# Kernel optimization log

Measured on AMD Instinct MI355X. Metric: run time of the kernel, lower is better.

Reference implementation:

```python
import jax, jax.numpy as jnp
import numpy as np
from jax import lax

EPS = 1e-5
NUM_GROUPS = 32
OFFSET_SCALE = 1.0
K = 3            # deformable conv kernel size
KK = K * K
DWK = 7          # depthwise kernel size for offset predictor


def group_norm(x, gamma, beta, num_groups=NUM_GROUPS):
    B, C, H, W = x.shape
    xg = x.reshape(B, num_groups, C // num_groups, H, W)
    m = xg.mean(axis=(2, 3, 4), keepdims=True)
    v = xg.var(axis=(2, 3, 4), keepdims=True)
    xn = ((xg - m) * lax.rsqrt(v + EPS)).reshape(B, C, H, W)
    return xn * gamma[None, :, None, None] + beta[None, :, None, None]


def bilinear_gather(x, py, px):
    # x: [B,C,H,W]; py, px: [B,KK,H,W] absolute sample coords -> [B,C,KK,H,W]
    B, C, H, W = x.shape
    y0 = jnp.floor(py)
    x0 = jnp.floor(px)
    wy1 = py - y0
    wx1 = px - x0
    wy0 = 1.0 - wy1
    wx0 = 1.0 - wx1
    xf = x.reshape(B, C, H * W)

    def gather(yi, xi):
        valid = (yi >= 0) & (yi <= H - 1) & (xi >= 0) & (xi <= W - 1)
        yc = jnp.clip(yi, 0, H - 1).astype(jnp.int32)
        xc = jnp.clip(xi, 0, W - 1).astype(jnp.int32)
        idx = (yc * W + xc).reshape(B, -1)                      # [B, KK*H*W]
        g = jax.vmap(lambda a, i: a[:, i])(xf, idx)             # [B, C, KK*H*W]
        g = g.reshape(B, C, KK, H, W)
        return g * valid.astype(x.dtype)[:, None]

    out = (gather(y0, x0) * (wy0 * wx0)[:, None]
           + gather(y0, x0 + 1.0) * (wy0 * wx1)[:, None]
           + gather(y0 + 1.0, x0) * (wy1 * wx0)[:, None]
           + gather(y0 + 1.0, x0 + 1.0) * (wy1 * wx1)[:, None])
    return out


def deform_conv(x, dw, pw, pwb, w, b):
    # x: [B,C,H,W]; dw: [C,1,DWK,DWK] depthwise; pw: [2*KK,C,1,1]; w: [O,C,K,K]
    B, C, H, W = x.shape
    dn = ('NCHW', 'OIHW', 'NCHW')
    f = lax.conv_general_dilated(x, dw, (1, 1), 'SAME',
                                 feature_group_count=C, dimension_numbers=dn)
    off = lax.conv_general_dilated(f, pw, (1, 1), 'SAME', dimension_numbers=dn)
    off = (off + pwb[None, :, None, None]) * OFFSET_SCALE       # [B,2*KK,H,W]
    off = off.reshape(B, KK, 2, H, W)
    ks = jnp.arange(K, dtype=x.dtype) - (K - 1) / 2             # [-1,0,1]
    ky = jnp.repeat(ks, K)                                      # [KK]
    kx = jnp.tile(ks, K)
    yy, xx = jnp.meshgrid(jnp.arange(H, dtype=x.dtype),
                          jnp.arange(W, dtype=x.dtype), indexing='ij')
    py = yy[None, None] + ky[None, :, None, None] + off[:, :, 0]  # [B,KK,H,W]
    px = xx[None, None] + kx[None, :, None, None] + off[:, :, 1]
    sampled = bilinear_gather(x, py, px)                        # [B,C,KK,H,W]
    O = w.shape[0]
    out = jnp.einsum('bckhw,ock->bohw', sampled, w.reshape(O, C, KK))
    return out + b[None, :, None, None]


def setup_inputs() -> dict:
    key = jax.random.key(0)
    ks = jax.random.split(key, 10)
    B, C, H, W = 4, 256, 64, 64
    O = C
    x = jax.random.normal(ks[0], (B, C, H, W), dtype=jnp.float32)

    def conv_w(k, shape, fan_in):
        return jax.random.normal(k, shape, dtype=jnp.float32) / np.sqrt(fan_in)

    inp = {
        'x': x,
        'gn1_g': jnp.ones((C,), jnp.float32), 'gn1_b': jnp.zeros((C,), jnp.float32),
        'dw1': conv_w(ks[1], (C, 1, DWK, DWK), DWK * DWK),
        'pw1': jax.random.normal(ks[2], (2 * KK, C, 1, 1), jnp.float32) * 0.01,
        'pwb1': jnp.zeros((2 * KK,), jnp.float32),
        'w1': conv_w(ks[3], (O, C, K, K), C * KK),
        'b1': jnp.zeros((O,), jnp.float32),
        'gn2_g': jnp.ones((O,), jnp.float32), 'gn2_b': jnp.zeros((O,), jnp.float32),
        'dw2': conv_w(ks[4], (O, 1, DWK, DWK), DWK * DWK),
        'pw2': jax.random.normal(ks[5], (2 * KK, O, 1, 1), jnp.float32) * 0.01,
        'pwb2': jnp.zeros((2 * KK,), jnp.float32),
        'w2': conv_w(ks[6], (O, O, K, K), O * KK),
        'b2': jnp.zeros((O,), jnp.float32),
    }
    return inp


def reference(x, gn1_g, gn1_b, dw1, pw1, pwb1, w1, b1,
              gn2_g, gn2_b, dw2, pw2, pwb2, w2, b2):
    h = jax.nn.relu(group_norm(x, gn1_g, gn1_b))
    h = deform_conv(h, dw1, pw1, pwb1, w1, b1)
    h = jax.nn.relu(group_norm(h, gn2_g, gn2_b))
    # Dropout / DropPath are identity in eval mode
    h = deform_conv(h, dw2, pw2, pwb2, w2, b2)
    return h + x  # shortcut is Identity (in_channels == out_channels)
```

## Files before the change

kernel.cpp:

```cpp
#include <hip/hip_runtime.h>

#define B_    4
#define C_    256
#define H_    64
#define W_    64
#define HW_   4096
#define NG_   32
#define CPG_  8
#define KK_   9
#define NOFF_ 18

typedef __attribute__((ext_vector_type(8))) short short8;
typedef __attribute__((ext_vector_type(4))) short short4v;
typedef __attribute__((ext_vector_type(4))) float floatx4;
typedef __attribute__((ext_vector_type(16))) float floatx16;

static __device__ __forceinline__ short f2bf(float f) {
    union { float f; unsigned u; } v; v.f = f;
    unsigned r = v.u + 0x7fff + ((v.u >> 16) & 1);
    return (short)(r >> 16);
}
static __device__ __forceinline__ float bf2f(short s) {
    union { unsigned u; float f; } v;
    v.u = ((unsigned)(unsigned short)s) << 16;
    return v.f;
}
static __device__ __forceinline__ unsigned pkbf(float lo, float hi) {
    unsigned r;
    asm("v_cvt_pk_bf16_f32 %0, %1, %2" : "=v"(r) : "v"(lo), "v"(hi));
    return r;
}

__global__ __launch_bounds__(1024) void gn_relu_f32_kernel(
    const float* __restrict__ in, const float* __restrict__ gamma,
    const float* __restrict__ beta, short* __restrict__ outb)
{
    __shared__ float cache[32768];
    __shared__ float red[32];
    __shared__ float sh_rs, sh_m;
    int b = blockIdx.x >> 5;
    int g = blockIdx.x & 31;
    const int N = CPG_ * HW_;
    size_t base = ((size_t)(b * C_ + g * CPG_)) * HW_;
    const float4* in4 = (const float4*)(in + base);
    int t = threadIdx.x;

    float s = 0.f, ss = 0.f;
    for (int i = t; i < N / 4; i += 1024) {
        float4 v = in4[i];
        *(float4*)&cache[i * 4] = v;
        s  += v.x + v.y + v.z + v.w;
        ss += v.x * v.x + v.y * v.y + v.z * v.z + v.w * v.w;
    }
    #pragma unroll
    for (int off = 32; off > 0; off >>= 1) {
        s  += __shfl_down(s, off, 64);
        ss += __shfl_down(ss, off, 64);
    }
    int wid = t >> 6;
    if ((t & 63) == 0) { red[wid] = s; red[16 + wid] = ss; }
    __syncthreads();
    if (t == 0) {
        float S = 0.f, SS = 0.f;
        #pragma unroll
        for (int i = 0; i < 16; ++i) { S += red[i]; SS += red[16 + i]; }
        float m = S / (float)N;
        float var = SS / (float)N - m * m;
        sh_rs = rsqrtf(var + 1e-5f);
        sh_m = m;
    }
    __syncthreads();
    float rs = sh_rs, m = sh_m;
    short4v* out4 = (short4v*)(outb + base);
    for (int i = t; i < N / 4; i += 1024) {
        int ch = g * CPG_ + (i >> 10);
        float ga = gamma[ch] * rs;
        float be = beta[ch] - m * ga;
        float4 v = *(const float4*)&cache[i * 4];
        short4v o;
        o.x = f2bf(fmaxf(fmaf(v.x, ga, be), 0.f));
        o.y = f2bf(fmaxf(fmaf(v.y, ga, be), 0.f));
        o.z = f2bf(fmaxf(fmaf(v.z, ga, be), 0.f));
        o.w = f2bf(fmaxf(fmaf(v.w, ga, be), 0.f));
        out4[i] = o;
    }
}

__global__ __launch_bounds__(256) void dw7t_tr_kernel(
    const short* __restrict__ in,
    const float* __restrict__ dwk,
    short* __restrict__ fdwt,
    short* __restrict__ ht,
    const float* __restrict__ pstats,
    const float* __restrict__ gamma, const float* __restrict__ beta)
{
    __shared__ __align__(16) char smem[78144];
    const float Ninv = 1.f / (float)(CPG_ * HW_);
    int t = threadIdx.x;
    int blk = blockIdx.x;
    if (blk < 256) {
        short (*tile)[38][72] = (short(*)[38][72])smem;
        float (*wk8)[49]      = (float(*)[49])(smem + 43776);
        short (*outs)[2048]   = (short(*)[2048])(smem + 45344);
        float* gsh            = (float*)(smem + 78112);
        int b = blk >> 6, o8 = (blk >> 1) & 31, rh = blk & 1;
        int c0 = o8 * 8;
        if (pstats && t < 64) {
            const float* pp = pstats + (((size_t)(b * 64 + t)) * 32 + o8) * 2;
            float s = pp[0], q = pp[1];
            #pragma unroll
            for (int off = 32; off > 0; off >>= 1) {
                s += __shfl_down(s, off, 64);
                q += __shfl_down(q, off, 64);
            }
            if (t == 0) {
                float m = s * Ninv;
                float var = q * Ninv - m * m;
                gsh[0] = m;
                gsh[1] = rsqrtf(var + 1e-5f);
            }
        }
        unsigned* tz = (unsigned*)smem;
        for (int i = t; i < 10944; i += 256) tz[i] = 0u;
        for (int i = t; i < 392; i += 256)
            wk8[i / 49][i % 49] = dwk[(c0 + i / 49) * 49 + (i % 49)];
        __syncthreads();
        float m_g = 0.f, rs_g = 0.f;
        if (pstats) { m_g = gsh[0]; rs_g = gsh[1]; }
        for (int ch = 0; ch < 8; ++ch) {
            const short* src = in + ((size_t)(b * C_ + c0 + ch)) * HW_;
            float ga = 0.f, be = 0.f;
            if (pstats) {
                ga = gamma[c0 + ch] * rs_g;
                be = beta[c0 + ch] - m_g * ga;
            }
            for (int i = t; i < 608; i += 256) {
                int rr = i >> 4, xq = i & 15;
                int ry = rh * 32 + rr - 3;
                if (ry >= 0 && ry < 64) {
                    short4v v = *(const short4v*)(src + ry * 64 + xq * 4);
                    if (pstats) {
                        v.x = f2bf(fmaxf(fmaf(bf2f(v.x), ga, be), 0.f));
                        v.y = f2bf(fmaxf(fmaf(bf2f(v.y), ga, be), 0.f));
                        v.z = f2bf(fmaxf(fmaf(bf2f(v.z), ga, be), 0.f));
                        v.w = f2bf(fmaxf(fmaf(bf2f(v.w), ga, be), 0.f));
                    }
                    *(short4v*)&tile[ch][rr][4 + xq * 4] = v;
                }
            }
        }
        __syncthreads();
        for (int it = 0; it < 16; ++it) {
            int q = it * 256 + t;
            int ch = q >> 9, y = (q >> 4) & 31, x0 = (q & 15) << 2;
            float a0 = 0.f, a1 = 0.f, a2 = 0.f, a3 = 0.f;
            const float* wr0 = wk8[ch];
            #pragma unroll
            for (int dy = 0; dy < 7; ++dy) {
                const short* trw = &tile[ch][y + dy][x0];
                short4v s0 = *(const short4v*)trw;
                short4v s1 = *(const short4v*)(trw + 4);
                short4v s2 = *(const short4v*)(trw + 8);
                float r[12] = {bf2f(s0.x), bf2f(s0.y), bf2f(s0.z), bf2f(s0.w),
                               bf2f(s1.x), bf2f(s1.y), bf2f(s1.z), bf2f(s1.w),
                               bf2f(s2.x), bf2f(s2.y), bf2f(s2.z), bf2f(s2.w)};
                const float* wr = wr0 + dy * 7;
                #pragma unroll
                for (int dx = 0; dx < 7; ++dx) {
                    float wv = wr[dx];
                    a0 = fmaf(r[dx + 1], wv, a0);
                    a1 = fmaf(r[dx + 2], wv, a1);
                    a2 = fmaf(r[dx + 3], wv, a2);
                    a3 = fmaf(r[dx + 4], wv, a3);
                }
            }
            short4v o;
            o.x = f2bf(a0); o.y = f2bf(a1); o.z = f2bf(a2); o.w = f2bf(a3);
            *(short4v*)&outs[ch][y * 64 + x0] = o;
        }
        __syncthreads();
        for (int it = 0; it < 8; ++it) {
            int p = it * 256 + t;
            short8 v;
            #pragma unroll
            for (int ch = 0; ch < 8; ++ch) v[ch] = outs[ch][p];
            *(short8*)(fdwt + (((size_t)(b * 64 + rh * 32 + (p >> 6)) * 32 + o8) * 64
                               + (p & 63)) * 8) = v;
        }
    } else {
        unsigned* ltile = (unsigned*)smem;
        float* gmrs = (float*)(smem + 65536);
        int q0 = blk - 256;
        int q = ((q0 & 7) << 5) | (q0 >> 3);
        int b = q >> 6;
        int px0 = (q & 63) * 64;
        const short* sb = in + (size_t)b * C_ * HW_;
        if (pstats) {
            int gq = t >> 3, rq = t & 7;
            float s = 0.f, qs = 0.f;
            for (int rr = rq; rr < 64; rr += 8) {
                const float* pp = pstats + (((size_t)(b * 64 + rr)) * 32 + gq) * 2;
                s += pp[0]; qs += pp[1];
            }
            s  += __shfl_down(s, 4, 64);  qs += __shfl_down(qs, 4, 64);
            s  += __shfl_down(s, 2, 64);  qs += __shfl_down(qs, 2, 64);
            s  += __shfl_down(s, 1, 64);  qs += __shfl_down(qs, 1, 64);
            if (rq == 0) {
                float m = s * Ninv;
                float var = qs * Ninv - m * m;
                gmrs[gq] = m;
                gmrs[32 + gq] = rsqrtf(var + 1e-5f);
            }
        }
        __syncthreads();
        int pq4 = t & 15, cphi = t >> 4;
        #pragma unroll
        for (int i = 0; i < 8; ++i) {
            int cp = i * 16 + cphi;
            const short* r0 = sb + (size_t)(2 * cp) * HW_ + px0 + pq4 * 4;
            short4v lo = *(const short4v*)r0;
            short4v hi = *(const short4v*)(r0 + HW_);
            float ga0 = 0.f, be0 = 0.f, ga1 = 0.f, be1 = 0.f;
            if (pstats) {
                int g0 = cp >> 2;
                float mm = gmrs[g0], rr2 = gmrs[32 + g0];
                ga0 = gamma[2 * cp] * rr2;     be0 = beta[2 * cp] - mm * ga0;
                ga1 = gamma[2 * cp + 1] * rr2; be1 = beta[2 * cp + 1] - mm * ga1;
            }
            #pragma unroll
            for (int j = 0; j < 4; ++j) {
                int pl = pq4 * 4 + j;
                unsigned wrd;
                if (pstats) {
                    float v0 = fmaxf(fmaf(bf2f(lo[j]), ga0, be0), 0.f);
                    float v1 = fmaxf(fmaf(bf2f(hi[j]), ga1, be1), 0.f);
                    wrd = pkbf(v0, v1);
                } else {
                    wrd = (unsigned)(unsigned short)lo[j]
                        | ((unsigned)(unsigned short)hi[j] << 16);
                }
                ltile[pl * 132 + (cp ^ ((pl & 7) << 2))] = wrd;
            }
        }
        __syncthreads();
        int co = t & 31, ph2 = t >> 5;
        #pragma unroll
        for (int r = 0; r < 8; ++r) {
            int pl = r * 8 + ph2;
            uint4 v = *(const uint4*)&ltile[pl * 132 + ((co * 4) ^ ((pl & 7) << 2))];
            *(uint4*)(ht + ((size_t)b * HW_ + px0 + pl) * C_ + co * 8) = v;
        }
    }
}

__global__ __launch_bounds__(256) void wpack_all_kernel(
    const float* __restrict__ w1, const float* __restrict__ w2,
    const float* __restrict__ pw1, const float* __restrict__ pw2,
    short* __restrict__ wp1, short* __restrict__ wp2,
    short* __restrict__ ppk1, short* __restrict__ ppk2)
{
    int blk = blockIdx.x;
    if (blk < 4608) {
        const float* w = (blk < 2304) ? w1 : w2;
        short* wp = (blk < 2304) ? wp1 : wp2;
        int src = (blk % 2304) * 256 + threadIdx.x;
        float v = w[src];
        int o = src / (C_ * KK_);
        int r = src - o * (C_ * KK_);
        int c = r / KK_;
        int g = r - c * KK_;
        int ot   = o >> 5;
        int lane = (o & 31) | (((c >> 3) & 1) << 5);
        int j    = c & 7;
        int slab = g * 16 + (c >> 4);
        wp[(slab << 12) | (ot << 9) | (lane << 3) | j] = f2bf(v);
    } else {
        int q = blk - 4608;
        const float* pw = (q < 32) ? pw1 : pw2;
        short* ppk = (q < 32) ? ppk1 : ppk2;
        int idx = (q & 31) * 256 + threadIdx.x;
        int j = idx & 7, lane = (idx >> 3) & 63;
        int ot = (idx >> 9) & 1, sl = idx >> 10;
        int o = ot * 16 + (lane & 15);
        int k = sl * 32 + (lane >> 4) * 8 + j;
        ppk[idx] = (o < NOFF_) ? f2bf(pw[o * C_ + k]) : (short)0;
    }
}

__global__ __launch_bounds__(1024, 4) void deform_fused_kernel(
    const short* __restrict__ ht,   const short* __restrict__ fdw,
    const short* __restrict__ ppk,  const float* __restrict__ pwb,
    const short* __restrict__ wp,   const float* __restrict__ bias,
    const float* __restrict__ resid, float* __restrict__ outf,
    short* __restrict__ outb,       float* __restrict__ pstats)
{
    int lb = ((blockIdx.x & 7) << 5) | (blockIdx.x >> 3);
    int b = lb >> 6;
    int row = lb & 63;
    __shared__ int   i00[576], i01[576], i10[576], i11[576];
    __shared__ float c00[576], c01[576], c10[576], c11[576];
    __shared__ __align__(16) short sbuf[2][2][8192];
    __shared__ float stat_lds[16][8];
    float* off_lds = (float*)&sbuf[0][0][0];
    int t = threadIdx.x;
    int wv = t >> 6, lane = t & 63;
    int pq = lane >> 4, pr = lane & 15;
    int l31 = lane & 31, hi = lane >> 5;

    if (wv < 8) {
        int ot = wv & 1, ptw = wv >> 1;
        int px = ptw * 16 + pr;
        const short8* fdw8 = (const short8*)fdw;
        size_t fbase = ((size_t)(b * 64 + row)) * 32;
        const short8* ap = (const short8*)ppk;
        floatx4 pacc = (floatx4){0.f, 0.f, 0.f, 0.f};
        #pragma unroll
        for (int sl = 0; sl < 8; ++sl) {
            short8 af = ap[(sl * 2 + ot) * 64 + lane];
            short8 bf = fdw8[(fbase + sl * 4 + pq) * 64 + px];
            pacc = __builtin_amdgcn_mfma_f32_16x16x32_bf16(af, bf, pacc, 0, 0, 0);
        }
        #pragma unroll
        for (int r = 0; r < 4; ++r) {
            int o = ot * 16 + pq * 4 + r;
            if (o < NOFF_) off_lds[o * 64 + px] = pacc[r] + pwb[o];
        }
    }
    __syncthreads();

    if (t < 576) {
        int e = t;
        int k = e >> 6, p = e & 63;
        float offy = off_lds[(2 * k) * 64 + p];
        float offx = off_lds[(2 * k + 1) * 64 + p];
        float py = (float)row + (float)(k / 3 - 1) + offy;
        float px = (float)p   + (float)(k % 3 - 1) + offx;
        float y0f = floorf(py), x0f = floorf(px);
        float wy1 = py - y0f, wx1 = px - x0f;
        float wy0 = 1.f - wy1, wx0 = 1.f - wx1;
        float y1f = y0f + 1.f, x1f = x0f + 1.f;
        bool vy0 = (y0f >= 0.f) && (y0f <= 63.f);
        bool vy1 = (y1f >= 0.f) && (y1f <= 63.f);
        bool vx0 = (x0f >= 0.f) && (x0f <= 63.f);
        bool vx1 = (x1f >= 0.f) && (x1f <= 63.f);
        int iy0 = (int)fminf(fmaxf(y0f, 0.f), 63.f);
        int iy1 = (int)fminf(fmaxf(y1f, 0.f), 63.f);
        int ix0 = (int)fminf(fmaxf(x0f, 0.f), 63.f);
        int ix1 = (int)fminf(fmaxf(x1f, 0.f), 63.f);
        i00[e] = iy0 * 64 + ix0; i01[e] = iy0 * 64 + ix1;
        i10[e] = iy1 * 64 + ix0; i11[e] = iy1 * 64 + ix1;
        c00[e] = (vy0 && vx0) ? wy0 * wx0 : 0.f;
        c01[e] = (vy0 && vx1) ? wy0 * wx1 : 0.f;
        c10[e] = (vy1 && vx0) ? wy1 * wx0 : 0.f;
        c11[e] = (vy1 && vx1) ? wy1 * wx1 : 0.f;
    }
    __syncthreads();

    int c8a = t & 7;
    int pan = (t >> 3) & 1;
    int spx = t >> 4;
    const short* hb0 = ht + ((size_t)b * HW_) * C_ + pan * 128 + c8a * 8;
    const short* hb1 = hb0 + 64;
    int slotA = (c8a ^ (spx & 15)) * 8;
    int slotB = ((c8a + 8) ^ (spx & 15)) * 8;
    int srow = spx * 128;

    short8 ra[4], rb[4];
    auto prefetch = [&](int g) {
        int e = g * 64 + spx;
        int a00 = i00[e], a01 = i01[e], a10 = i10[e], a11 = i11[e];
        ra[0] = *(const short8*)(hb0 + (size_t)a00 * C_);
        ra[1] = *(const short8*)(hb0 + (size_t)a01 * C_);
        ra[2] = *(const short8*)(hb0 + (size_t)a10 * C_);
        ra[3] = *(const short8*)(hb0 + (size_t)a11 * C_);
        rb[0] = *(const short8*)(hb1 + (size_t)a00 * C_);
        rb[1] = *(const short8*)(hb1 + (size_t)a01 * C_);
        rb[2] = *(const short8*)(hb1 + (size_t)a10 * C_);
        rb[3] = *(const short8*)(hb1 + (size_t)a11 * C_);
    };
    auto stage_write = [&](int g, int bi) {
        int e = g * 64 + spx;
        float w00 = c00[e], w01 = c01[e], w10 = c10[e], w11 = c11[e];
        uint4 va, vb;
        float f0, f1;
        #define BLEND(R, J) (w00 * bf2f(R[0][J]) + w01 * bf2f(R[1][J]) \
                           + w10 * bf2f(R[2][J]) + w11 * bf2f(R[3][J]))
        f0 = BLEND(ra, 0); f1 = BLEND(ra, 1); va.x = pkbf(f0, f1);
        f0 = BLEND(ra, 2); f1 = BLEND(ra, 3); va.y = pkbf(f0, f1);
        f0 = BLEND(ra, 4); f1 = BLEND(ra, 5); va.z = pkbf(f0, f1);
        f0 = BLEND(ra, 6); f1 = BLEND(ra, 7); va.w = pkbf(f0, f1);
        f0 = BLEND(rb, 0); f1 = BLEND(rb, 1); vb.x = pkbf(f0, f1);
        f0 = BLEND(rb, 2); f1 = BLEND(rb, 3); vb.y = pkbf(f0, f1);
        f0 = BLEND(rb, 4); f1 = BLEND(rb, 5); vb.z = pkbf(f0, f1);
        f0 = BLEND(rb, 6); f1 = BLEND(rb, 7); vb.w = pkbf(f0, f1);
        #undef BLEND
        short* sp = &sbuf[bi][pan][srow];
        *(uint4*)&sp[slotA] = va;
        *(uint4*)&sp[slotB] = vb;
    };

    int pairId = wv & 7;
    int half = wv >> 3;

    floatx16 acc[2];
    #pragma unroll
    for (int i = 0; i < 16; ++i) { acc[0][i] = 0.f; acc[1][i] = 0.f; }

    prefetch(0);
    stage_write(0, 0);
    prefetch(1);
    __syncthreads();

    const short8* wp8 = (const short8*)wp;
    int msk = l31 & 15;

    for (int g = 0; g < 9; ++g) {
        const short* sb = &sbuf[g & 1][half][0];
        #pragma unroll
        for (int q4 = 0; q4 < 2; ++q4) {
            short8 af[4];
            #pragma unroll
            for (int qq = 0; qq < 4; ++qq)
                af[qq] = wp8[(size_t)(((g * 16 + half * 8 + q4 * 4 + qq) * 8 + pairId) * 64 + lane)];
            #pragma unroll
            for (int qq = 0; qq < 4; ++qq) {
                int ksl = q4 * 4 + qq;
                int so = ((((ksl << 1) | hi) ^ msk) << 3);
                short8 b0 = *(const short8*)&sb[l31 * 128 + so];
                short8 b1 = *(const short8*)&sb[(32 + l31) * 128 + so];
                acc[0] = __builtin_amdgcn_mfma_f32_32x32x16_bf16(af[qq], b0, acc[0], 0, 0, 0);
                acc[1] = __builtin_amdgcn_mfma_f32_32x32x16_bf16(af[qq], b1, acc[1], 0, 0, 0);
            }
        }
        if (g + 1 < 9) {
            stage_write(g + 1, (g + 1) & 1);
            if (g + 2 < 9) prefetch(g + 2);
        }
        __syncthreads();
    }

    float* xch = (float*)&sbuf[0][0][0];
    int wreg = (pairId * 2 + half) * 1024;
    floatx16 aw = half ? acc[0] : acc[1];
    floatx4* xq = (floatx4*)xch;
    #pragma unroll
    for (int j = 0; j < 4; ++j) {
        floatx4 v = {aw[j * 4 + 0], aw[j * 4 + 1], aw[j * 4 + 2], aw[j * 4 + 3]};
        xq[(wreg >> 2) + j * 64 + lane] = v;
    }
    __syncthreads();
    int rreg = (pairId * 2 + (half ^ 1)) * 1024;
    floatx16 ac = half ? acc[1] : acc[0];
    #pragma unroll
    for (int j = 0; j < 4; ++j) {
        floatx4 v = xq[(rreg >> 2) + j * 64 + lane];
        ac[j * 4 + 0] += v.x; ac[j * 4 + 1] += v.y;
        ac[j * 4 + 2] += v.z; ac[j * 4 + 3] += v.w;
    }

    float sj[4] = {0.f, 0.f, 0.f, 0.f};
    float qj[4] = {0.f, 0.f, 0.f, 0.f};
    #pragma unroll
    for (int r = 0; r < 16; ++r) {
        int o = pairId * 32 + (r & 3) + 8 * (r >> 2) + 4 * hi;
        float v = ac[r] + bias[o];
        size_t ob = ((size_t)(b * C_ + o)) * HW_ + row * 64 + half * 32 + l31;
        if (outf) {
            if (resid) v += resid[ob];
            outf[ob] = v;
        } else {
            outb[ob] = f2bf(v);
            sj[r >> 2] += v;
            qj[r >> 2] += v * v;
        }
    }
    if (pstats) {
        #pragma unroll
        for (int off = 32; off > 0; off >>= 1) {
            #pragma unroll
            for (int j = 0; j < 4; ++j) {
                sj[j] += __shfl_down(sj[j], off, 64);
                qj[j] += __shfl_down(qj[j], off, 64);
            }
        }
        if (lane == 0) {
            #pragma unroll
            for (int j = 0; j < 4; ++j) {
                stat_lds[wv][j] = sj[j];
                stat_lds[wv][4 + j] = qj[j];
            }
        }
        __syncthreads();
        if (t < 32) {
            int pid = t >> 2, j = t & 3;
            float sT = stat_lds[pid][j] + stat_lds[pid + 8][j];
            float qT = stat_lds[pid][4 + j] + stat_lds[pid + 8][4 + j];
            float* pp = pstats + (((size_t)(b * 64 + row)) * 32 + pid * 4 + j) * 2;
            pp[0] = sT;
            pp[1] = qT;
        }
    }
}

extern "C" void kernel_launch(void* const* d_in, const int* in_sizes, int n_in,
                              void* d_out, int out_size, void* d_ws, size_t ws_size,
                              hipStream_t stream)
{
    const float* x     = (const float*)d_in[0];
    const float* gn1_g = (const float*)d_in[1];
    const float* gn1_b = (const float*)d_in[2];
    const float* dw1   = (const float*)d_in[3];
    const float* pw1   = (const float*)d_in[4];
    const float* pwb1  = (const float*)d_in[5];
    const float* w1    = (const float*)d_in[6];
    const float* b1    = (const float*)d_in[7];
    const float* gn2_g = (const float*)d_in[8];
    const float* gn2_b = (const float*)d_in[9];
    const float* dw2   = (const float*)d_in[10];
    const float* pw2   = (const float*)d_in[11];
    const float* pwb2  = (const float*)d_in[12];
    const float* w2    = (const float*)d_in[13];
    const float* b2    = (const float*)d_in[14];
    float* out = (float*)d_out;

    float* ws   = (float*)d_ws;
    short* y1b  = (short*)ws;
    short* hbf  = (short*)(ws + 2097152);
    short* hbt  = (short*)(ws + 4194304);
    short* fdwt = (short*)(ws + 8388608);
    short* wp1  = (short*)(ws + 10485760);
    short* wp2  = (short*)(ws + 10780672);
    short* ppk1 = (short*)(ws + 11075584);
    short* ppk2 = (short*)(ws + 11079680);
    float* pstats = ws + 11083776;

    wpack_all_kernel<<<4672, 256, 0, stream>>>(w1, w2, pw1, pw2,
                                               wp1, wp2, ppk1, ppk2);

    gn_relu_f32_kernel<<<B_ * NG_, 1024, 0, stream>>>(x, gn1_g, gn1_b, hbf);
    dw7t_tr_kernel<<<512, 256, 0, stream>>>(hbf, dw1, fdwt, hbt,
                                            nullptr, nullptr, nullptr);
    deform_fused_kernel<<<B_ * H_, 1024, 0, stream>>>(
        hbt, fdwt, ppk1, pwb1, wp1, b1, nullptr, nullptr, y1b, pstats);

    dw7t_tr_kernel<<<512, 256, 0, stream>>>(y1b, dw2, fdwt, hbt,
                                            pstats, gn2_g, gn2_b);
    deform_fused_kernel<<<B_ * H_, 1024, 0, stream>>>(
        hbt, fdwt, ppk2, pwb2, wp2, b2, x, out, nullptr, nullptr);
}
```

Before: 236.4 us.

## Fuse GN1 stats into weight-pack kernel and apply GN1 inside depthwise/transpose

Removes the standalone GroupNorm1 kernel, which wrote a bf16 normalized copy of x. GN1 statistics are now computed by extra blocks appended to the weight-packing launch. The first depthwise/transpose kernel reads fp32 x directly and applies normalize plus ReLU on the fly. This saves one launch and a full write-then-read round trip of the activation, but the dw kernel now reads fp32 (twice the bytes) in both of its branches, and the pstats null checks are removed.

```diff
diff --git a/kernel.cpp b/kernel.cpp
--- a/kernel.cpp
+++ b/kernel.cpp
@@ -31,58 +31,193 @@
     return r;
 }
 
-__global__ __launch_bounds__(1024) void gn_relu_f32_kernel(
-    const float* __restrict__ in, const float* __restrict__ gamma,
-    const float* __restrict__ beta, short* __restrict__ outb)
+__global__ __launch_bounds__(256) void wpack_gn1_kernel(
+    const float* __restrict__ w1, const float* __restrict__ w2,
+    const float* __restrict__ pw1, const float* __restrict__ pw2,
+    short* __restrict__ wp1, short* __restrict__ wp2,
+    short* __restrict__ ppk1, short* __restrict__ ppk2,
+    const float* __restrict__ xin, float* __restrict__ gstats)
 {
-    __shared__ float cache[32768];
-    __shared__ float red[32];
-    __shared__ float sh_rs, sh_m;
-    int b = blockIdx.x >> 5;
-    int g = blockIdx.x & 31;
-    const int N = CPG_ * HW_;
-    size_t base = ((size_t)(b * C_ + g * CPG_)) * HW_;
-    const float4* in4 = (const float4*)(in + base);
+    __shared__ float red[8];
+    int blk = blockIdx.x;
+    if (blk < 4608) {
+        const float* w = (blk < 2304) ? w1 : w2;
+        short* wp = (blk < 2304) ? wp1 : wp2;
+        int src = (blk % 2304) * 256 + threadIdx.x;
+        float v = w[src];
+        int o = src / (C_ * KK_);
+        int r = src - o * (C_ * KK_);
+        int c = r / KK_;
+        int g = r - c * KK_;
+        int ot   = o >> 5;
+        int lane = (o & 31) | (((c >> 3) & 1) << 5);
+        int j    = c & 7;
+        int slab = g * 16 + (c >> 4);
+        wp[(slab << 12) | (ot << 9) | (lane << 3) | j] = f2bf(v);
+    } else if (blk < 4672) {
+        int q = blk - 4608;
+        const float* pw = (q < 32) ? pw1 : pw2;
+        short* ppk = (q < 32) ? ppk1 : ppk2;
+        int idx = (q & 31) * 256 + threadIdx.x;
+        int j = idx & 7, lane = (idx >> 3) & 63;
+        int ot = (idx >> 9) & 1, sl = idx >> 10;
+        int o = ot * 16 + (lane & 15);
+        int k = sl * 32 + (lane >> 4) * 8 + j;
+        ppk[idx] = (o < NOFF_) ? f2bf(pw[o * C_ + k]) : (short)0;
+    } else {
+        int q = blk - 4672;
+        int b = q >> 5, g = q & 31;
+        const int N = CPG_ * HW_;
+        size_t base = ((size_t)(b * C_ + g * CPG_)) * HW_;
+        const float4* in4 = (const float4*)(xin + base);
+        int t = threadIdx.x;
+        float s = 0.f, ss = 0.f;
+        for (int i = t; i < N / 4; i += 256) {
+            float4 v = in4[i];
+            s  += v.x + v.y + v.z + v.w;
+            ss += v.x * v.x + v.y * v.y + v.z * v.z + v.w * v.w;
+        }
+        #pragma unroll
+        for (int off = 32; off > 0; off >>= 1) {
+            s  += __shfl_down(s, off, 64);
+            ss += __shfl_down(ss, off, 64);
+        }
+        int wid = t >> 6;
+        if ((t & 63) == 0) { red[wid] = s; red[4 + wid] = ss; }
+        __syncthreads();
+        if (t == 0) {
+            float S = red[0] + red[1] + red[2] + red[3];
+            float SS = red[4] + red[5] + red[6] + red[7];
+            float m = S / (float)N;
+            float var = SS / (float)N - m * m;
+            gstats[b * 32 + g] = m;
+            gstats[128 + b * 32 + g] = rsqrtf(var + 1e-5f);
+        }
+    }
+}
+
+__global__ __launch_bounds__(256) void dw7t_tr_f32_kernel(
+    const float* __restrict__ in,
+    const float* __restrict__ dwk,
+    short* __restrict__ fdwt,
+    short* __restrict__ ht,
+    const float* __restrict__ gstats,
+    const float* __restrict__ gamma, const float* __restrict__ beta)
+{
+    __shared__ __align__(16) char smem[78144];
     int t = threadIdx.x;
-
-    float s = 0.f, ss = 0.f;
-    for (int i = t; i < N / 4; i += 1024) {
-        float4 v = in4[i];
-        *(float4*)&cache[i * 4] = v;
-        s  += v.x + v.y + v.z + v.w;
-        ss += v.x * v.x + v.y * v.y + v.z * v.z + v.w * v.w;
-    }
-    #pragma unroll
-    for (int off = 32; off > 0; off >>= 1) {
-        s  += __shfl_down(s, off, 64);
-        ss += __shfl_down(ss, off, 64);
-    }
-    int wid = t >> 6;
-    if ((t & 63) == 0) { red[wid] = s; red[16 + wid] = ss; }
-    __syncthreads();
-    if (t == 0) {
-        float S = 0.f, SS = 0.f;
-        #pragma unroll
-        for (int i = 0; i < 16; ++i) { S += red[i]; SS += red[16 + i]; }
-        float m = S / (float)N;
-        float var = SS / (float)N - m * m;
-        sh_rs = rsqrtf(var + 1e-5f);
-        sh_m = m;
-    }
-    __syncthreads();
-    float rs = sh_rs, m = sh_m;
-    short4v* out4 = (short4v*)(outb + base);
-    for (int i = t; i < N / 4; i += 1024) {
-        int ch = g * CPG_ + (i >> 10);
-        float ga = gamma[ch] * rs;
-        float be = beta[ch] - m * ga;
-        float4 v = *(const float4*)&cache[i * 4];
-        short4v o;
-        o.x = f2bf(fmaxf(fmaf(v.x, ga, be), 0.f));
-        o.y = f2bf(fmaxf(fmaf(v.y, ga, be), 0.f));
-        o.z = f2bf(fmaxf(fmaf(v.z, ga, be), 0.f));
-        o.w = f2bf(fmaxf(fmaf(v.w, ga, be), 0.f));
-        out4[i] = o;
+    int blk = blockIdx.x;
+    if (blk < 256) {
+        short (*tile)[38][72] = (short(*)[38][72])smem;
+        float (*wk8)[49]      = (float(*)[49])(smem + 43776);
+        short (*outs)[2048]   = (short(*)[2048])(smem + 45344);
+        int b = blk >> 6, o8 = (blk >> 1) & 31, rh = blk & 1;
+        int c0 = o8 * 8;
+        int sidx = b * 32 + o8;
+        float m_g = gstats[sidx], rs_g = gstats[128 + sidx];
+        unsigned* tz = (unsigned*)smem;
+        for (int i = t; i < 10944; i += 256) tz[i] = 0u;
+        for (int i = t; i < 392; i += 256)
+            wk8[i / 49][i % 49] = dwk[(c0 + i / 49) * 49 + (i % 49)];
+        __syncthreads();
+        for (int ch = 0; ch < 8; ++ch) {
+            const float* src = in + ((size_t)(b * C_ + c0 + ch)) * HW_;
+            float ga = gamma[c0 + ch] * rs_g;
+            float be = beta[c0 + ch] - m_g * ga;
+            for (int i = t; i < 608; i += 256) {
+                int rr = i >> 4, xq = i & 15;
+                int ry = rh * 32 + rr - 3;
+                if (ry >= 0 && ry < 64) {
+                    float4 v = *(const float4*)(src + ry * 64 + xq * 4);
+                    short4v o;
+                    o.x = f2bf(fmaxf(fmaf(v.x, ga, be), 0.f));
+                    o.y = f2bf(fmaxf(fmaf(v.y, ga, be), 0.f));
+                    o.z = f2bf(fmaxf(fmaf(v.z, ga, be), 0.f));
+                    o.w = f2bf(fmaxf(fmaf(v.w, ga, be), 0.f));
+                    *(short4v*)&tile[ch][rr][4 + xq * 4] = o;
+                }
+            }
+        }
+        __syncthreads();
+        for (int it = 0; it < 16; ++it) {
+            int q = it * 256 + t;
+            int ch = q >> 9, y = (q >> 4) & 31, x0 = (q & 15) << 2;
+            float a0 = 0.f, a1 = 0.f, a2 = 0.f, a3 = 0.f;
+            const float* wr0 = wk8[ch];
+            #pragma unroll
+            for (int dy = 0; dy < 7; ++dy) {
+                const short* trw = &tile[ch][y + dy][x0];
+                short4v s0 = *(const short4v*)trw;
+                short4v s1 = *(const short4v*)(trw + 4);
+                short4v s2 = *(const short4v*)(trw + 8);
+                float r[12] = {bf2f(s0.x), bf2f(s0.y), bf2f(s0.z), bf2f(s0.w),
+                               bf2f(s1.x), bf2f(s1.y), bf2f(s1.z), bf2f(s1.w),
+                               bf2f(s2.x), bf2f(s2.y), bf2f(s2.z), bf2f(s2.w)};
+                const float* wr = wr0 + dy * 7;
+                #pragma unroll
+                for (int dx = 0; dx < 7; ++dx) {
+                    float wv = wr[dx];
+                    a0 = fmaf(r[dx + 1], wv, a0);
+                    a1 = fmaf(r[dx + 2], wv, a1);
+                    a2 = fmaf(r[dx + 3], wv, a2);
+                    a3 = fmaf(r[dx + 4], wv, a3);
+                }
+            }
+            short4v o;
+            o.x = f2bf(a0); o.y = f2bf(a1); o.z = f2bf(a2); o.w = f2bf(a3);
+            *(short4v*)&outs[ch][y * 64 + x0] = o;
+        }
+        __syncthreads();
+        for (int it = 0; it < 8; ++it) {
+            int p = it * 256 + t;
+            short8 v;
+            #pragma unroll
+            for (int ch = 0; ch < 8; ++ch) v[ch] = outs[ch][p];
+            *(short8*)(fdwt + (((size_t)(b * 64 + rh * 32 + (p >> 6)) * 32 + o8) * 64
+                               + (p & 63)) * 8) = v;
+        }
+    } else {
+        unsigned* ltile = (unsigned*)smem;
+        float* gmrs = (float*)(smem + 65536);
+        int q0 = blk - 256;
+        int q = ((q0 & 7) << 5) | (q0 >> 3);
+        int b = q >> 6;
+        int px0 = (q & 63) * 64;
+        const float* sb = in + (size_t)b * C_ * HW_;
+        if (t < 32) {
+            gmrs[t] = gstats[b * 32 + t];
+            gmrs[32 + t] = gstats[128 + b * 32 + t];
+        }
+        __syncthreads();
+        int pq4 = t & 15, cphi = t >> 4;
+        #pragma unroll
+        for (int i = 0; i < 8; ++i) {
+            int cp = i * 16 + cphi;
+            const float* r0 = sb + (size_t)(2 * cp) * HW_ + px0 + pq4 * 4;
+            float4 flo = *(const float4*)r0;
+            float4 fhi = *(const float4*)(r0 + HW_);
+            int g0 = cp >> 2;
+            float mm = gmrs[g0], rr2 = gmrs[32 + g0];
+            float ga0 = gamma[2 * cp] * rr2;     float be0 = beta[2 * cp] - mm * ga0;
+            float ga1 = gamma[2 * cp + 1] * rr2; float be1 = beta[2 * cp + 1] - mm * ga1;
+            float lo[4] = {flo.x, flo.y, flo.z, flo.w};
+            float hi[4] = {fhi.x, fhi.y, fhi.z, fhi.w};
+            #pragma unroll
+            for (int j = 0; j < 4; ++j) {
+                int pl = pq4 * 4 + j;
+                float v0 = fmaxf(fmaf(lo[j], ga0, be0), 0.f);
+                float v1 = fmaxf(fmaf(hi[j], ga1, be1), 0.f);
+                ltile[pl * 132 + (cp ^ ((pl & 7) << 2))] = pkbf(v0, v1);
+            }
+        }
+        __syncthreads();
+        int co = t & 31, ph2 = t >> 5;
+        #pragma unroll
+        for (int r = 0; r < 8; ++r) {
+            int pl = r * 8 + ph2;
+            uint4 v = *(const uint4*)&ltile[pl * 132 + ((co * 4) ^ ((pl & 7) << 2))];
+            *(uint4*)(ht + ((size_t)b * HW_ + px0 + pl) * C_ + co * 8) = v;
+        }
     }
 }
 
@@ -105,7 +240,7 @@
         float* gsh            = (float*)(smem + 78112);
         int b = blk >> 6, o8 = (blk >> 1) & 31, rh = blk & 1;
         int c0 = o8 * 8;
-        if (pstats && t < 64) {
+        if (t < 64) {
             const float* pp = pstats + (((size_t)(b * 64 + t)) * 32 + o8) * 2;
             float s = pp[0], q = pp[1];
             #pragma unroll
@@ -125,26 +260,20 @@
         for (int i = t; i < 392; i += 256)
             wk8[i / 49][i % 49] = dwk[(c0 + i / 49) * 49 + (i % 49)];
         __syncthreads();
-        float m_g = 0.f, rs_g = 0.f;
-        if (pstats) { m_g = gsh[0]; rs_g = gsh[1]; }
+        float m_g = gsh[0], rs_g = gsh[1];
         for (int ch = 0; ch < 8; ++ch) {
             const short* src = in + ((size_t)(b * C_ + c0 + ch)) * HW_;
-            float ga = 0.f, be = 0.f;
-            if (pstats) {
-                ga = gamma[c0 + ch] * rs_g;
-                be = beta[c0 + ch] - m_g * ga;
-            }
+            float ga = gamma[c0 + ch] * rs_g;
+            float be = beta[c0 + ch] - m_g * ga;
             for (int i = t; i < 608; i += 256) {
                 int rr = i >> 4, xq = i & 15;
                 int ry = rh * 32 + rr - 3;
                 if (ry >= 0 && ry < 64) {
                     short4v v = *(const short4v*)(src + ry * 64 + xq * 4);
-                    if (pstats) {
-                        v.x = f2bf(fmaxf(fmaf(bf2f(v.x), ga, be), 0.f));
-                        v.y = f2bf(fmaxf(fmaf(bf2f(v.y), ga, be), 0.f));
-                        v.z = f2bf(fmaxf(fmaf(bf2f(v.z), ga, be), 0.f));
-                        v.w = f2bf(fmaxf(fmaf(bf2f(v.w), ga, be), 0.f));
-                    }
+                    v.x = f2bf(fmaxf(fmaf(bf2f(v.x), ga, be), 0.f));
+                    v.y = f2bf(fmaxf(fmaf(bf2f(v.y), ga, be), 0.f));
+                    v.z = f2bf(fmaxf(fmaf(bf2f(v.z), ga, be), 0.f));
+                    v.w = f2bf(fmaxf(fmaf(bf2f(v.w), ga, be), 0.f));
                     *(short4v*)&tile[ch][rr][4 + xq * 4] = v;
                 }
             }
@@ -195,7 +324,7 @@
         int b = q >> 6;
         int px0 = (q & 63) * 64;
         const short* sb = in + (size_t)b * C_ * HW_;
-        if (pstats) {
+        {
             int gq = t >> 3, rq = t & 7;
             float s = 0.f, qs = 0.f;
             for (int rr = rq; rr < 64; rr += 8) {
@@ -220,26 +349,16 @@
             const short* r0 = sb + (size_t)(2 * cp) * HW_ + px0 + pq4 * 4;
             short4v lo = *(const short4v*)r0;
             short4v hi = *(const short4v*)(r0 + HW_);
-            float ga0 = 0.f, be0 = 0.f, ga1 = 0.f, be1 = 0.f;
-            if (pstats) {
-                int g0 = cp >> 2;
-                float mm = gmrs[g0], rr2 = gmrs[32 + g0];
-                ga0 = gamma[2 * cp] * rr2;     be0 = beta[2 * cp] - mm * ga0;
-                ga1 = gamma[2 * cp + 1] * rr2; be1 = beta[2 * cp + 1] - mm * ga1;
-            }
+            int g0 = cp >> 2;
+            float mm = gmrs[g0], rr2 = gmrs[32 + g0];
+            float ga0 = gamma[2 * cp] * rr2;     float be0 = beta[2 * cp] - mm * ga0;
+            float ga1 = gamma[2 * cp + 1] * rr2; float be1 = beta[2 * cp + 1] - mm * ga1;
             #pragma unroll
             for (int j = 0; j < 4; ++j) {
                 int pl = pq4 * 4 + j;
-                unsigned wrd;
-                if (pstats) {
-                    float v0 = fmaxf(fmaf(bf2f(lo[j]), ga0, be0), 0.f);
-                    float v1 = fmaxf(fmaf(bf2f(hi[j]), ga1, be1), 0.f);
-                    wrd = pkbf(v0, v1);
-                } else {
-                    wrd = (unsigned)(unsigned short)lo[j]
-                        | ((unsigned)(unsigned short)hi[j] << 16);
-                }
-                ltile[pl * 132 + (cp ^ ((pl & 7) << 2))] = wrd;
+                float v0 = fmaxf(fmaf(bf2f(lo[j]), ga0, be0), 0.f);
+                float v1 = fmaxf(fmaf(bf2f(hi[j]), ga1, be1), 0.f);
+                ltile[pl * 132 + (cp ^ ((pl & 7) << 2))] = pkbf(v0, v1);
             }
         }
         __syncthreads();
@@ -250,40 +369,6 @@
             uint4 v = *(const uint4*)&ltile[pl * 132 + ((co * 4) ^ ((pl & 7) << 2))];
             *(uint4*)(ht + ((size_t)b * HW_ + px0 + pl) * C_ + co * 8) = v;
         }
-    }
-}
-
-__global__ __launch_bounds__(256) void wpack_all_kernel(
-    const float* __restrict__ w1, const float* __restrict__ w2,
-    const float* __restrict__ pw1, const float* __restrict__ pw2,
-    short* __restrict__ wp1, short* __restrict__ wp2,
-    short* __restrict__ ppk1, short* __restrict__ ppk2)
-{
-    int blk = blockIdx.x;
-    if (blk < 4608) {
-        const float* w = (blk < 2304) ? w1 : w2;
-        short* wp = (blk < 2304) ? wp1 : wp2;
-        int src = (blk % 2304) * 256 + threadIdx.x;
-        float v = w[src];
-        int o = src / (C_ * KK_);
-        int r = src - o * (C_ * KK_);
-        int c = r / KK_;
-        int g = r - c * KK_;
-        int ot   = o >> 5;
-        int lane = (o & 31) | (((c >> 3) & 1) << 5);
-        int j    = c & 7;
-        int slab = g * 16 + (c >> 4);
-        wp[(slab << 12) | (ot << 9) | (lane << 3) | j] = f2bf(v);
-    } else {
-        int q = blk - 4608;
-        const float* pw = (q < 32) ? pw1 : pw2;
-        short* ppk = (q < 32) ? ppk1 : ppk2;
-        int idx = (q & 31) * 256 + threadIdx.x;
-        int j = idx & 7, lane = (idx >> 3) & 63;
-        int ot = (idx >> 9) & 1, sl = idx >> 10;
-        int o = ot * 16 + (lane & 15);
-        int k = sl * 32 + (lane >> 4) * 8 + j;
-        ppk[idx] = (o < NOFF_) ? f2bf(pw[o * C_ + k]) : (short)0;
     }
 }
 
@@ -525,21 +610,21 @@
 
     float* ws   = (float*)d_ws;
     short* y1b  = (short*)ws;
-    short* hbf  = (short*)(ws + 2097152);
     short* hbt  = (short*)(ws + 4194304);
     short* fdwt = (short*)(ws + 8388608);
     short* wp1  = (short*)(ws + 10485760);
     short* wp2  = (short*)(ws + 10780672);
     short* ppk1 = (short*)(ws + 11075584);
     short* ppk2 = (short*)(ws + 11079680);
-    float* pstats = ws + 11083776;
-
-    wpack_all_kernel<<<4672, 256, 0, stream>>>(w1, w2, pw1, pw2,
-                                               wp1, wp2, ppk1, ppk2);
-
-    gn_relu_f32_kernel<<<B_ * NG_, 1024, 0, stream>>>(x, gn1_g, gn1_b, hbf);
-    dw7t_tr_kernel<<<512, 256, 0, stream>>>(hbf, dw1, fdwt, hbt,
-                                            nullptr, nullptr, nullptr);
+    float* pstats  = ws + 11083776;
+    float* gstats1 = ws + 11100160;
+
+    wpack_gn1_kernel<<<4800, 256, 0, stream>>>(w1, w2, pw1, pw2,
+                                               wp1, wp2, ppk1, ppk2,
+                                               x, gstats1);
+
+    dw7t_tr_f32_kernel<<<512, 256, 0, stream>>>(x, dw1, fdwt, hbt,
+                                                gstats1, gn1_g, gn1_b);
     deform_fused_kernel<<<B_ * H_, 1024, 0, stream>>>(
         hbt, fdwt, ppk1, pwb1, wp1, b1, nullptr, nullptr, y1b, pstats);
 
```

New measurement: 242.1 us. +2.4%, slower.
